# Optimization experiments

Hardware: AMD Instinct MI355X
Metric: run time of the kernel (lower is better)

Reference implementation:

```python
import jax, jax.numpy as jnp
import numpy as np

POS_WEIGHT = 2.0
NEG_POS_RATIO = 20
EMPTY_NEG_RATIO = 0.01  # implemented as num_neg // 100 (== int(num_neg * 0.01))
POS_FRAC = 0.02  # sparse positives so the OHEM top-k path is exercised


def setup_inputs() -> dict:
    key = jax.random.key(0)
    k1, k2 = jax.random.split(key)
    logits = jax.random.normal(k1, (32, 2, 1024, 1024), dtype=jnp.float32)
    target = (jax.random.uniform(k2, (32, 1024, 1024)) < POS_FRAC).astype(jnp.float32)
    pos_weight = jnp.float32(POS_WEIGHT)
    return {"logits": logits, "target": target, "pos_weight": pos_weight}


def reference(logits, target, pos_weight):
    # channel slice: keep class-1 logit -> [B,1,H,W]
    x = logits[:, 1:2, :, :]
    t = target[:, None, :, :]  # [B,1,H,W]

    # BCEWithLogits(pos_weight): pw*t*softplus(-x) + (1-t)*softplus(x)
    bce = pos_weight * t * jax.nn.softplus(-x) + (1.0 - t) * jax.nn.softplus(x)

    pos_mask = t > 0.5
    n_total = bce.size
    num_pos = jnp.sum(pos_mask).astype(jnp.int32)
    num_neg = jnp.int32(n_total) - num_pos

    # mean over positive pixels (0 if none)
    pos_sum = jnp.sum(jnp.where(pos_mask, bce, 0.0))
    pos_keep = jnp.where(num_pos > 0,
                         pos_sum / jnp.maximum(num_pos, 1).astype(bce.dtype),
                         jnp.array(0.0, bce.dtype))

    # hard-negative mining: sort negatives descending (positives pushed below
    # all real bce values, which are >= 0, by filling with -1)
    NEG_FILL = jnp.array(-1.0, bce.dtype)
    neg_vals = jnp.where(pos_mask, NEG_FILL, bce).ravel()
    neg_sorted = jnp.sort(neg_vals)[::-1]

    k = jnp.where(num_pos > 0,
                  jnp.minimum(num_neg, NEG_POS_RATIO * num_pos),
                  jnp.maximum(jnp.int32(1), num_neg // 100))

    ranks = jnp.arange(n_total, dtype=jnp.int32)
    kept = ranks < k  # top-k hardest negatives (k <= num_neg when num_neg > 0)
    neg_sum = jnp.sum(jnp.where(kept, neg_sorted, 0.0))
    neg_keep = jnp.where(num_neg > 0,
                         neg_sum / jnp.maximum(k, 1).astype(bce.dtype),
                         jnp.array(0.0, bce.dtype))

    return pos_keep + neg_keep
```

## Files before the change

kernel.cpp:

```cpp
#include <hip/hip_runtime.h>


#define HW_SHIFT 20
#define HW_MASK  ((1 << HW_SHIFT) - 1)
#define NBINS 4096
#define NCOPY 8
#define NBLK 1024
#define SCALE 16384.0f
#define INV_SCALE (1.0 / 16384.0)

__device__ __forceinline__ float softplus_fast(float x) {
  return fmaxf(x, 0.0f) + __logf(1.0f + __expf(-fabsf(x)));
}

__device__ __forceinline__ unsigned keymap(float x) {
  unsigned b = __float_as_uint(x);
  unsigned m = (unsigned)((int)b >> 31);
  return b ^ (m | 0x80000000u);
}

__global__ void __launch_bounds__(256) p1_kernel(
    const float* __restrict__ logits, const float* __restrict__ target,
    unsigned long long* __restrict__ gsum,
    unsigned* __restrict__ ghist,
    unsigned* __restrict__ pcnt,
    double* __restrict__ psum,
    int nGroups) {
  __shared__ unsigned long long lhist[NBINS + 1];
  for (int i = threadIdx.x; i < NBINS + 1; i += 256) lhist[i] = 0ull;
  __syncthreads();

  const int lane = threadIdx.x & 63;
  const int wid = threadIdx.x >> 6;
  const int idx = blockIdx.x * 256 + threadIdx.x;
  const int stride = gridDim.x * 256;
  const int e0 = idx << 2;
  const int b0 = e0 >> HW_SHIFT;
  const int inner = e0 & HW_MASK;
  const float* lp = logits + (((size_t)b0) << (HW_SHIFT + 1)) + (1u << HW_SHIFT) + inner;
  const float* tp = target + (((size_t)b0) << HW_SHIFT) + inner;
  const size_t tAdv = (size_t)stride << 2;
  const size_t lAdv = (size_t)(stride >> (HW_SHIFT - 2)) << (HW_SHIFT + 1);

  unsigned posCnt = 0;
  float posSum = 0.0f;
  for (int g = idx; g < nGroups; g += stride) {
    const float4 xv = *reinterpret_cast<const float4*>(lp);
    const float4 tv = *reinterpret_cast<const float4*>(tp);
    const float xs[4] = {xv.x, xv.y, xv.z, xv.w};
    const float ts[4] = {tv.x, tv.y, tv.z, tv.w};
#pragma unroll
    for (int j = 0; j < 4; ++j) {
      const float x = xs[j], t = ts[j];
      const bool pos = t > 0.5f;
      const float sp = softplus_fast(x);
      posSum = __builtin_fmaf(t, sp - x, posSum);
      posCnt += pos ? 1u : 0u;
      const unsigned bin = pos ? (unsigned)NBINS : (keymap(x) >> 20);
      const unsigned su = (unsigned)__builtin_fmaf(sp, SCALE, 0.5f);
      atomicAdd(&lhist[bin], 0x0001000000000000ull | (unsigned long long)su);
    }
    lp += lAdv;
    tp += tAdv;
  }
  __syncthreads();

  const unsigned copy = blockIdx.x & (NCOPY - 1);
  unsigned long long* gs = gsum + (size_t)copy * NBINS;
  unsigned* gh = ghist + (size_t)copy * NBINS;
  const unsigned rot = (unsigned)(blockIdx.x << 6);
  for (int i = threadIdx.x; i < NBINS; i += 256) {
    const unsigned b = (i + rot) & (NBINS - 1);
    const unsigned long long v = lhist[b];
    if (v) {
      atomicAdd(&gh[b], (unsigned)(v >> 48));
      atomicAdd(&gs[b], v & 0x0000FFFFFFFFFFFFull);
    }
  }

#pragma unroll
  for (int o = 32; o; o >>= 1) {
    posCnt += __shfl_down(posCnt, o, 64);
    posSum += __shfl_down(posSum, o, 64);
  }
  __shared__ unsigned wpc[4];
  __shared__ float wps[4];
  if (lane == 0) { wpc[wid] = posCnt; wps[wid] = posSum; }
  __syncthreads();
  if (threadIdx.x == 0) {
    pcnt[blockIdx.x] = wpc[0] + wpc[1] + wpc[2] + wpc[3];
    psum[blockIdx.x] = (double)wps[0] + (double)wps[1] + (double)wps[2] + (double)wps[3];
  }
}

__global__ void __launch_bounds__(256) s1_kernel(
    const unsigned long long* __restrict__ gsum, const unsigned* __restrict__ ghist,
    const unsigned* __restrict__ pcnt, const double* __restrict__ psum,
    const float* __restrict__ pwPtr, float* __restrict__ out, int nTotal) {
  const int tid = threadIdx.x;

  unsigned pc = 0;
  double ps = 0.0;
  for (int i = tid; i < NBLK; i += 256) { pc += pcnt[i]; ps += psum[i]; }
  __shared__ unsigned spc[256];
  __shared__ double sps[256];
  spc[tid] = pc; sps[tid] = ps;
  __syncthreads();
  for (int o = 128; o; o >>= 1) {
    if (tid < o) { spc[tid] += spc[tid + o]; sps[tid] += sps[tid + o]; }
    __syncthreads();
  }
  const unsigned numPos = spc[0];
  const double posSum = sps[0];
  __syncthreads();

  unsigned cv[16];
  double sv[16];
  unsigned cS = 0;
  double sS = 0.0;
#pragma unroll
  for (int j = 0; j < 16; ++j) {
    const int bin = tid * 16 + j;
    unsigned c = 0;
    unsigned long long s = 0ull;
#pragma unroll
    for (int cp = 0; cp < NCOPY; ++cp) {
      c += ghist[cp * NBINS + bin];
      s += gsum[cp * NBINS + bin];
    }
    cv[j] = c;
    sv[j] = (double)s * INV_SCALE;
    cS += c;
    sS += sv[j];
  }
  __shared__ unsigned cChunk[256];
  __shared__ double sChunk[256];
  cChunk[tid] = cS; sChunk[tid] = sS;
  __syncthreads();
  unsigned cumAboveC = 0;
  double cumAboveS = 0.0;
  for (int j = tid + 1; j < 256; ++j) {
    cumAboveC += cChunk[j];
    cumAboveS += sChunk[j];
  }

  const unsigned numNeg = (unsigned)nTotal - numPos;
  unsigned k = (numPos > 0) ? min(numNeg, 20u * numPos) : max(1u, numNeg / 100u);
  if (numNeg == 0) k = 0;
  const double posKeep = (numPos > 0) ? ((double)pwPtr[0] * posSum / (double)numPos) : 0.0;
  if (k == 0) {
    if (tid == 0) out[0] = (float)posKeep;
    return;
  }
  if (cumAboveC < k && k <= cumAboveC + cS) {
    unsigned c = cumAboveC;
    double s = cumAboveS;
#pragma unroll
    for (int j = 15; j >= 0; --j) {
      if (c + cv[j] >= k) {
        const unsigned r2 = k - c;
        const double mean = sv[j] / (double)cv[j];
        const double negSum = s + (double)r2 * mean;
        out[0] = (float)(posKeep + negSum / (double)k);
        break;
      }
      c += cv[j];
      s += sv[j];
    }
  }
}

extern "C" void kernel_launch(void* const* d_in, const int* in_sizes, int n_in,
                              void* d_out, int out_size, void* d_ws, size_t ws_size,
                              hipStream_t stream) {
  const float* logits = (const float*)d_in[0];
  const float* target = (const float*)d_in[1];
  const float* pw = (const float*)d_in[2];
  float* out = (float*)d_out;

  const int nTotal = in_sizes[1];
  const int nGroups = nTotal >> 2;

  char* ws = (char*)d_ws;
  unsigned long long* gsum = (unsigned long long*)ws;
  unsigned* ghist = (unsigned*)(ws + 262144);
  unsigned* pcnt = (unsigned*)(ws + 393216);
  double* psum = (double*)(ws + 397312);

  hipMemsetAsync(d_ws, 0, 393216, stream);
  p1_kernel<<<NBLK, 256, 0, stream>>>(logits, target, gsum, ghist, pcnt, psum, nGroups);
  s1_kernel<<<1, 256, 0, stream>>>(gsum, ghist, pcnt, psum, pw, out, nTotal);
}
```

Baseline: 79.25 us.

## Fuse histogram and selection kernels with last-block ticket finalization

Merges the histogram pass and the single-block top-k selection into one kernel. The last block to finish, found through an atomic ticket, performs the final scan. Positive count and sum now come from the extra histogram bin instead of separate per-block reductions. The change also uses 512 threads per block, 4 global histogram copies instead of 8, an unrolled fixed-trip main loop with a tail loop, and a smaller memset. This removes a kernel launch and the per-block partial-sum traffic, at the cost of more global atomic contention per copy and a serialized tail in the last block.

```diff
diff --git a/kernel.cpp b/kernel.cpp
--- a/kernel.cpp
+++ b/kernel.cpp
@@ -4,9 +4,10 @@
 #define HW_SHIFT 20
 #define HW_MASK  ((1 << HW_SHIFT) - 1)
 #define NBINS 4096
-#define NCOPY 8
+#define NCOPY 4
 #define NBLK 1024
-#define SCALE 16384.0f
+#define NTHR 512
+#define SCALEF 16384.0f
 #define INV_SCALE (1.0 / 16384.0)
 
 __device__ __forceinline__ float softplus_fast(float x) {
@@ -19,149 +20,159 @@
   return b ^ (m | 0x80000000u);
 }
 
-__global__ void __launch_bounds__(256) p1_kernel(
+__global__ void __launch_bounds__(NTHR, 8) fused_kernel(
     const float* __restrict__ logits, const float* __restrict__ target,
     unsigned long long* __restrict__ gsum,
-    unsigned* __restrict__ ghist,
-    unsigned* __restrict__ pcnt,
-    double* __restrict__ psum,
-    int nGroups) {
+    unsigned* __restrict__ gcnt,
+    unsigned* __restrict__ ticket,
+    const float* __restrict__ pwPtr, float* __restrict__ out, int nTotal) {
   __shared__ unsigned long long lhist[NBINS + 1];
-  for (int i = threadIdx.x; i < NBINS + 1; i += 256) lhist[i] = 0ull;
-  __syncthreads();
-
-  const int lane = threadIdx.x & 63;
-  const int wid = threadIdx.x >> 6;
-  const int idx = blockIdx.x * 256 + threadIdx.x;
-  const int stride = gridDim.x * 256;
+  for (int i = threadIdx.x; i <= NBINS; i += NTHR) lhist[i] = 0ull;
+  __syncthreads();
+
+  const int idx = blockIdx.x * NTHR + threadIdx.x;
+  const int step = NBLK * NTHR * 4;
   const int e0 = idx << 2;
-  const int b0 = e0 >> HW_SHIFT;
-  const int inner = e0 & HW_MASK;
-  const float* lp = logits + (((size_t)b0) << (HW_SHIFT + 1)) + (1u << HW_SHIFT) + inner;
-  const float* tp = target + (((size_t)b0) << HW_SHIFT) + inner;
-  const size_t tAdv = (size_t)stride << 2;
-  const size_t lAdv = (size_t)(stride >> (HW_SHIFT - 2)) << (HW_SHIFT + 1);
-
-  unsigned posCnt = 0;
-  float posSum = 0.0f;
-  for (int g = idx; g < nGroups; g += stride) {
-    const float4 xv = *reinterpret_cast<const float4*>(lp);
-    const float4 tv = *reinterpret_cast<const float4*>(tp);
-    const float xs[4] = {xv.x, xv.y, xv.z, xv.w};
-    const float ts[4] = {tv.x, tv.y, tv.z, tv.w};
+  const int nFull = nTotal / step;
+  {
+    const int b0 = e0 >> HW_SHIFT;
+    const int inner = e0 & HW_MASK;
+    const float* lp = logits + (((size_t)b0) << (HW_SHIFT + 1)) + (1u << HW_SHIFT) + inner;
+    const float* tp = target + (((size_t)b0) << HW_SHIFT) + inner;
+    const size_t lAdv = ((size_t)(step >> HW_SHIFT)) << (HW_SHIFT + 1);
+    const size_t tAdv = (size_t)step;
+#pragma unroll 2
+    for (int it = 0; it < nFull; ++it) {
+      const float4 xv = *reinterpret_cast<const float4*>(lp);
+      const float4 tv = *reinterpret_cast<const float4*>(tp);
+      const float xs[4] = {xv.x, xv.y, xv.z, xv.w};
+      const float ts[4] = {tv.x, tv.y, tv.z, tv.w};
+#pragma unroll
+      for (int j = 0; j < 4; ++j) {
+        const float x = xs[j];
+        const bool pos = ts[j] > 0.5f;
+        const float sp = softplus_fast(x);
+        const float val = pos ? (sp - x) : sp;
+        const unsigned bin = pos ? (unsigned)NBINS : (keymap(x) >> 20);
+        const unsigned su = (unsigned)__builtin_fmaf(val, SCALEF, 0.5f);
+        atomicAdd(&lhist[bin], 0x0001000000000000ull | (unsigned long long)su);
+      }
+      lp += lAdv;
+      tp += tAdv;
+    }
+  }
+  for (int e = e0 + nFull * step; e < nTotal; e += step) {
 #pragma unroll
     for (int j = 0; j < 4; ++j) {
-      const float x = xs[j], t = ts[j];
-      const bool pos = t > 0.5f;
-      const float sp = softplus_fast(x);
-      posSum = __builtin_fmaf(t, sp - x, posSum);
-      posCnt += pos ? 1u : 0u;
-      const unsigned bin = pos ? (unsigned)NBINS : (keymap(x) >> 20);
-      const unsigned su = (unsigned)__builtin_fmaf(sp, SCALE, 0.5f);
-      atomicAdd(&lhist[bin], 0x0001000000000000ull | (unsigned long long)su);
-    }
-    lp += lAdv;
-    tp += tAdv;
-  }
-  __syncthreads();
-
-  const unsigned copy = blockIdx.x & (NCOPY - 1);
-  unsigned long long* gs = gsum + (size_t)copy * NBINS;
-  unsigned* gh = ghist + (size_t)copy * NBINS;
-  const unsigned rot = (unsigned)(blockIdx.x << 6);
-  for (int i = threadIdx.x; i < NBINS; i += 256) {
-    const unsigned b = (i + rot) & (NBINS - 1);
-    const unsigned long long v = lhist[b];
-    if (v) {
-      atomicAdd(&gh[b], (unsigned)(v >> 48));
-      atomicAdd(&gs[b], v & 0x0000FFFFFFFFFFFFull);
-    }
-  }
-
-#pragma unroll
-  for (int o = 32; o; o >>= 1) {
-    posCnt += __shfl_down(posCnt, o, 64);
-    posSum += __shfl_down(posSum, o, 64);
-  }
-  __shared__ unsigned wpc[4];
-  __shared__ float wps[4];
-  if (lane == 0) { wpc[wid] = posCnt; wps[wid] = posSum; }
-  __syncthreads();
-  if (threadIdx.x == 0) {
-    pcnt[blockIdx.x] = wpc[0] + wpc[1] + wpc[2] + wpc[3];
-    psum[blockIdx.x] = (double)wps[0] + (double)wps[1] + (double)wps[2] + (double)wps[3];
-  }
-}
-
-__global__ void __launch_bounds__(256) s1_kernel(
-    const unsigned long long* __restrict__ gsum, const unsigned* __restrict__ ghist,
-    const unsigned* __restrict__ pcnt, const double* __restrict__ psum,
-    const float* __restrict__ pwPtr, float* __restrict__ out, int nTotal) {
+      const int ei = e + j;
+      if (ei < nTotal) {
+        const int b = ei >> HW_SHIFT;
+        const int inner = ei & HW_MASK;
+        const float x = logits[(((size_t)b) << (HW_SHIFT + 1)) + (1u << HW_SHIFT) + inner];
+        const bool pos = target[ei] > 0.5f;
+        const float sp = softplus_fast(x);
+        const float val = pos ? (sp - x) : sp;
+        const unsigned bin = pos ? (unsigned)NBINS : (keymap(x) >> 20);
+        const unsigned su = (unsigned)__builtin_fmaf(val, SCALEF, 0.5f);
+        atomicAdd(&lhist[bin], 0x0001000000000000ull | (unsigned long long)su);
+      }
+    }
+  }
+  __syncthreads();
+
+  {
+    const size_t cp = (size_t)(blockIdx.x & (NCOPY - 1)) * (NBINS + 1);
+    unsigned long long* gs = gsum + cp;
+    unsigned* gc = gcnt + cp;
+    const unsigned rot = (blockIdx.x * 977u) & (NBINS - 1);
+    for (int i = threadIdx.x; i <= NBINS; i += NTHR) {
+      const unsigned b = (i < NBINS) ? ((i + rot) & (NBINS - 1)) : (unsigned)NBINS;
+      const unsigned long long v = lhist[b];
+      if (v) {
+        atomicAdd(&gc[b], (unsigned)(v >> 48));
+        atomicAdd(&gs[b], v & 0x0000FFFFFFFFFFFFull);
+      }
+    }
+  }
+  __threadfence();
+
+  __shared__ bool amLast;
+  if (threadIdx.x == 0)
+    amLast = (atomicAdd(ticket, 1u) == (unsigned)(gridDim.x - 1));
+  __syncthreads();
+  if (!amLast) return;
+  __threadfence();
+
   const int tid = threadIdx.x;
-
-  unsigned pc = 0;
-  double ps = 0.0;
-  for (int i = tid; i < NBLK; i += 256) { pc += pcnt[i]; ps += psum[i]; }
-  __shared__ unsigned spc[256];
-  __shared__ double sps[256];
-  spc[tid] = pc; sps[tid] = ps;
-  __syncthreads();
-  for (int o = 128; o; o >>= 1) {
-    if (tid < o) { spc[tid] += spc[tid + o]; sps[tid] += sps[tid + o]; }
-    __syncthreads();
-  }
-  const unsigned numPos = spc[0];
-  const double posSum = sps[0];
-  __syncthreads();
-
-  unsigned cv[16];
-  double sv[16];
+  __shared__ double posSum_s;
+  __shared__ unsigned posCnt_s;
+  if (tid == 0) {
+    unsigned c = 0;
+    unsigned long long s = 0ull;
+#pragma unroll
+    for (int cp = 0; cp < NCOPY; ++cp) {
+      c += __hip_atomic_load(&gcnt[(size_t)cp * (NBINS + 1) + NBINS],
+                             __ATOMIC_RELAXED, __HIP_MEMORY_SCOPE_AGENT);
+      s += __hip_atomic_load(&gsum[(size_t)cp * (NBINS + 1) + NBINS],
+                             __ATOMIC_RELAXED, __HIP_MEMORY_SCOPE_AGENT);
+    }
+    posCnt_s = c;
+    posSum_s = (double)s * INV_SCALE;
+  }
+
+  constexpr int BPT = NBINS / NTHR;
+  unsigned cv[BPT];
+  double sv[BPT];
   unsigned cS = 0;
   double sS = 0.0;
 #pragma unroll
-  for (int j = 0; j < 16; ++j) {
-    const int bin = tid * 16 + j;
+  for (int j = 0; j < BPT; ++j) {
+    const int bin = tid * BPT + j;
     unsigned c = 0;
     unsigned long long s = 0ull;
 #pragma unroll
     for (int cp = 0; cp < NCOPY; ++cp) {
-      c += ghist[cp * NBINS + bin];
-      s += gsum[cp * NBINS + bin];
+      c += __hip_atomic_load(&gcnt[(size_t)cp * (NBINS + 1) + bin],
+                             __ATOMIC_RELAXED, __HIP_MEMORY_SCOPE_AGENT);
+      s += __hip_atomic_load(&gsum[(size_t)cp * (NBINS + 1) + bin],
+                             __ATOMIC_RELAXED, __HIP_MEMORY_SCOPE_AGENT);
     }
     cv[j] = c;
     sv[j] = (double)s * INV_SCALE;
     cS += c;
     sS += sv[j];
   }
-  __shared__ unsigned cChunk[256];
-  __shared__ double sChunk[256];
-  cChunk[tid] = cS; sChunk[tid] = sS;
-  __syncthreads();
-  unsigned cumAboveC = 0;
-  double cumAboveS = 0.0;
-  for (int j = tid + 1; j < 256; ++j) {
-    cumAboveC += cChunk[j];
-    cumAboveS += sChunk[j];
-  }
-
+  __shared__ unsigned cChunk[NTHR];
+  __shared__ double sChunk[NTHR];
+  cChunk[tid] = cS;
+  sChunk[tid] = sS;
+  __syncthreads();
+  unsigned cumC = 0;
+  double cumS = 0.0;
+  for (int j = tid + 1; j < NTHR; ++j) {
+    cumC += cChunk[j];
+    cumS += sChunk[j];
+  }
+
+  const unsigned numPos = posCnt_s;
   const unsigned numNeg = (unsigned)nTotal - numPos;
   unsigned k = (numPos > 0) ? min(numNeg, 20u * numPos) : max(1u, numNeg / 100u);
   if (numNeg == 0) k = 0;
-  const double posKeep = (numPos > 0) ? ((double)pwPtr[0] * posSum / (double)numPos) : 0.0;
+  const double posKeep =
+      (numPos > 0) ? ((double)pwPtr[0] * posSum_s / (double)numPos) : 0.0;
   if (k == 0) {
     if (tid == 0) out[0] = (float)posKeep;
     return;
   }
-  if (cumAboveC < k && k <= cumAboveC + cS) {
-    unsigned c = cumAboveC;
-    double s = cumAboveS;
-#pragma unroll
-    for (int j = 15; j >= 0; --j) {
+  if (cumC < k && k <= cumC + cS) {
+    unsigned c = cumC;
+    double s = cumS;
+#pragma unroll
+    for (int j = BPT - 1; j >= 0; --j) {
       if (c + cv[j] >= k) {
         const unsigned r2 = k - c;
         const double mean = sv[j] / (double)cv[j];
-        const double negSum = s + (double)r2 * mean;
-        out[0] = (float)(posKeep + negSum / (double)k);
+        out[0] = (float)(posKeep + (s + (double)r2 * mean) / (double)k);
         break;
       }
       c += cv[j];
@@ -179,15 +190,13 @@
   float* out = (float*)d_out;
 
   const int nTotal = in_sizes[1];
-  const int nGroups = nTotal >> 2;
 
   char* ws = (char*)d_ws;
   unsigned long long* gsum = (unsigned long long*)ws;
-  unsigned* ghist = (unsigned*)(ws + 262144);
-  unsigned* pcnt = (unsigned*)(ws + 393216);
-  double* psum = (double*)(ws + 397312);
-
-  hipMemsetAsync(d_ws, 0, 393216, stream);
-  p1_kernel<<<NBLK, 256, 0, stream>>>(logits, target, gsum, ghist, pcnt, psum, nGroups);
-  s1_kernel<<<1, 256, 0, stream>>>(gsum, ghist, pcnt, psum, pw, out, nTotal);
-}
+  unsigned* gcnt = (unsigned*)(ws + 131104);
+  unsigned* ticket = (unsigned*)(ws + 131104 + 65552);
+
+  hipMemsetAsync(d_ws, 0, 131104 + 65552 + 4, stream);
+  fused_kernel<<<NBLK, NTHR, 0, stream>>>(logits, target, gsum, gcnt, ticket,
+                                          pw, out, nTotal);
+}
```

Measured after the change: 264.2 us. 3.33x slower.
